# Kernel optimization log

Hardware: AMD Instinct MI355X
Metric: run time of the kernel (lower is better)

Reference implementation:

```python
import jax, jax.numpy as jnp
import numpy as np

V, D = 100000, 300          # fastText vocab / dim
CV, CD, L = 128, 16, 16     # char vocab / char emb dim / word length
F = 50                      # filters per kernel
KS = (3, 4, 5)              # char CNN kernel widths
H = 150                     # LSTM hidden per direction (2H == D)
FH = 150                    # alpha-encoder FFNN hidden
NF, FE = 64, 50             # entity feature vocab / dim
A = 2000                    # num actors
T = 1024                    # tokens
E = 512                     # entity spans
MAXSPAN = 10                # max span length (ragged -> padded+masked)


def setup_inputs() -> dict:
    key = jax.random.key(0)
    ks = jax.random.split(key, 24)
    g = lambda i, shape, s=0.05: jax.random.normal(ks[i], shape, jnp.float32) * s
    inp = {}
    inp['fast_text'] = g(0, (V, D), 0.1)
    inp['actor_matrix'] = g(1, (A, D), 0.1)
    inp['char_table'] = g(2, (CV, CD), 0.1)
    for j, k in enumerate(KS):
        inp[f'conv_w{k}'] = g(3 + j, (F, CD, k))
        inp[f'conv_b{k}'] = jnp.zeros((F,), jnp.float32)
    din = D + F * len(KS)  # 450 = fastText + char features
    inp['Wi_f'] = g(6, (4 * H, din)); inp['Wh_f'] = g(7, (4 * H, H)); inp['b_f'] = jnp.zeros((4 * H,), jnp.float32)
    inp['Wi_b'] = g(8, (4 * H, din)); inp['Wh_b'] = g(9, (4 * H, H)); inp['b_b'] = jnp.zeros((4 * H,), jnp.float32)
    inp['alpha_W1'] = g(10, (D, FH)); inp['alpha_b1'] = jnp.zeros((FH,), jnp.float32)
    inp['alpha_W2'] = g(11, (FH, FH)); inp['alpha_b2'] = jnp.zeros((FH,), jnp.float32)
    inp['alpha_w_out'] = g(12, (FH,))
    inp['feat_table'] = g(13, (NF, FE), 0.1)
    span_dim = 3 * D + 2 * FE  # 1000, per Model1.span_encoding_dim
    inp['affine_W'] = g(14, (span_dim, D)); inp['affine_b'] = jnp.zeros((D,), jnp.float32)
    inp['word_ids'] = jax.random.randint(ks[15], (T,), 0, V)
    inp['char_ids'] = jax.random.randint(ks[16], (T, L), 0, CV)
    starts = jax.random.randint(ks[17], (E,), 0, T - MAXSPAN)
    lens = jax.random.randint(ks[18], (E,), 1, MAXSPAN + 1)
    feats = jax.random.randint(ks[19], (E, 2), 0, NF)
    inp['espans'] = jnp.concatenate([starts[:, None], (starts + lens)[:, None], feats], axis=1)
    return inp


def _renorm(e):
    # nn.Embedding(max_norm=1.0): renormalize looked-up rows to L2 norm <= 1
    n = jnp.linalg.norm(e, axis=-1, keepdims=True)
    return e * jnp.minimum(1.0, 1.0 / jnp.maximum(n, 1e-7))


def _lstm(x, Wi, Wh, b, reverse):
    Hh = Wh.shape[1]
    def step(carry, xt):
        h, c = carry
        z = xt @ Wi.T + h @ Wh.T + b
        i, f, g2, o = jnp.split(z, 4)
        i = jax.nn.sigmoid(i); f = jax.nn.sigmoid(f)
        g2 = jnp.tanh(g2); o = jax.nn.sigmoid(o)
        c = f * c + i * g2
        h = o * jnp.tanh(c)
        return (h, c), h
    init = (jnp.zeros((Hh,), x.dtype), jnp.zeros((Hh,), x.dtype))
    _, hs = jax.lax.scan(step, init, x, reverse=reverse)
    return hs  # [T, H], hs[i] corresponds to position i


def reference(fast_text, actor_matrix, char_table, conv_w3, conv_b3, conv_w4, conv_b4,
              conv_w5, conv_b5, Wi_f, Wh_f, b_f, Wi_b, Wh_b, b_b,
              alpha_W1, alpha_b1, alpha_W2, alpha_b2, alpha_w_out,
              feat_table, affine_W, affine_b, word_ids, char_ids, espans):
    # --- WordEncoder: fastText + char CNN -> BiLSTM contextual embeddings ---
    ft = fast_text[word_ids]                       # [T, D] fastText embeddings (values)
    ce = char_table[char_ids]                      # [T, L, CD]
    xc = jnp.transpose(ce, (0, 2, 1))              # [T, CD, L]
    feats = []
    for w, bb in ((conv_w3, conv_b3), (conv_w4, conv_b4), (conv_w5, conv_b5)):
        y = jax.lax.conv_general_dilated(xc, w, (1,), 'VALID',
                                         dimension_numbers=('NCW', 'OIW', 'NCW'))
        feats.append(jnp.max(jax.nn.relu(y + bb[None, :, None]), axis=-1))  # [T, F]
    char_feat = jnp.concatenate(feats, axis=-1)    # [T, 150]
    lstm_in = jnp.concatenate([ft, char_feat], axis=-1)  # [T, 450]
    h_f = _lstm(lstm_in, Wi_f, Wh_f, b_f, False)
    h_b = _lstm(lstm_in, Wi_b, Wh_b, b_b, True)
    keys = jnp.concatenate([h_f, h_b], axis=-1)    # [T, D] contextual word embeddings
    values = ft

    # --- espan_encodings: ragged span gather, padded + masked, fully vectorized ---
    s, e = espans[:, 0], espans[:, 1]
    fidx = espans[:, 2:]                           # [E, 2]
    offs = jnp.arange(MAXSPAN)
    idx = jnp.clip(s[:, None] + offs[None, :], 0, keys.shape[0] - 1)  # [E, S]
    mask = offs[None, :] < (e - s)[:, None]        # [E, S]
    k_sp = keys[idx]                               # [E, S, D]
    v_sp = values[idx]                             # [E, S, D]
    # SingleQueryEncoder (alpha_encoder): FFNN scores over keys, softmax-pool values
    hsc = jax.nn.relu(k_sp @ alpha_W1 + alpha_b1)
    hsc = jax.nn.relu(hsc @ alpha_W2 + alpha_b2)
    logits = jnp.where(mask, hsc @ alpha_w_out, -1e30)  # [E, S]
    attn = jax.nn.softmax(logits, axis=-1)
    xh = jnp.einsum('es,esd->ed', attn, v_sp)      # [E, D]
    xf = keys[s]                                   # first token
    xl = keys[e - 1]                               # last token
    fs = _renorm(feat_table[fidx]).reshape(fidx.shape[0], -1)  # [E, 2*FE]
    enc = jnp.concatenate([xf, xl, xh, fs], axis=-1)  # [E, 3D+2FE]

    small = enc @ affine_W + affine_b              # [E, D] affine_ent
    actors = _renorm(actor_matrix)                 # [A, D] actor_embedding max_norm=1
    score_link = actors @ small.T                  # [A, E] DotProduct.simpel
    score_1 = jax.nn.logsumexp(score_link, axis=1) # [A]   Maximum.lse over dim=1
    return score_1, score_link
```

## Files before the change

kernel.cpp:

```cpp
#include <hip/hip_runtime.h>
#include <math.h>

typedef _Float16 h2f __attribute__((ext_vector_type(2)));

__device__ __forceinline__ float fdot2f(h2f a, h2f b, float c) {
#if __has_builtin(__builtin_amdgcn_fdot2)
  return __builtin_amdgcn_fdot2(a, b, c, false);
#else
  return c + (float)a[0] * (float)b[0] + (float)a[1] * (float)b[1];
#endif
}

__device__ __forceinline__ float sigf(float x) {
  return __builtin_amdgcn_rcpf(1.f + __expf(-x));
}
__device__ __forceinline__ float tanh_fast(float x) {
  return 2.f * __builtin_amdgcn_rcpf(1.f + __expf(-2.f * x)) - 1.f;
}

__device__ __forceinline__ int clampi(int v, int lo, int hi) {
  return v < lo ? lo : (v > hi ? hi : v);
}

__global__ __launch_bounds__(64) void k_token(
    const float* __restrict__ fast_text, const float* __restrict__ char_table,
    const float* __restrict__ w3, const float* __restrict__ b3,
    const float* __restrict__ w4, const float* __restrict__ b4,
    const float* __restrict__ w5, const float* __restrict__ b5,
    const int* __restrict__ word_ids, const int* __restrict__ char_ids,
    float* __restrict__ lstm_in) {
  const int t = blockIdx.x;
  const int tid = threadIdx.x;
  __shared__ float ce[16][16];
  for (int i = tid; i < 256; i += 64) {
    int l = i >> 4, ci = i & 15;
    ce[l][ci] = char_table[char_ids[t * 16 + l] * 16 + ci];
  }
  __syncthreads();
  const int wid = word_ids[t];
  for (int d = tid; d < 300; d += 64)
    lstm_in[t * 450 + d] = fast_text[wid * 300 + d];
  const int f = tid;
  if (f < 50) {
    {
      float acc[14];
#pragma unroll
      for (int p = 0; p < 14; ++p) acc[p] = 0.f;
      for (int ci = 0; ci < 16; ++ci) {
#pragma unroll
        for (int kk = 0; kk < 3; ++kk) {
          float wv = w3[(f * 16 + ci) * 3 + kk];
#pragma unroll
          for (int p = 0; p < 14; ++p) acc[p] += ce[p + kk][ci] * wv;
        }
      }
      float m = acc[0];
#pragma unroll
      for (int p = 1; p < 14; ++p) m = fmaxf(m, acc[p]);
      lstm_in[t * 450 + 300 + f] = fmaxf(0.f, m + b3[f]);
    }
    {
      float acc[13];
#pragma unroll
      for (int p = 0; p < 13; ++p) acc[p] = 0.f;
      for (int ci = 0; ci < 16; ++ci) {
#pragma unroll
        for (int kk = 0; kk < 4; ++kk) {
          float wv = w4[(f * 16 + ci) * 4 + kk];
#pragma unroll
          for (int p = 0; p < 13; ++p) acc[p] += ce[p + kk][ci] * wv;
        }
      }
      float m = acc[0];
#pragma unroll
      for (int p = 1; p < 13; ++p) m = fmaxf(m, acc[p]);
      lstm_in[t * 450 + 350 + f] = fmaxf(0.f, m + b4[f]);
    }
    {
      float acc[12];
#pragma unroll
      for (int p = 0; p < 12; ++p) acc[p] = 0.f;
      for (int ci = 0; ci < 16; ++ci) {
#pragma unroll
        for (int kk = 0; kk < 5; ++kk) {
          float wv = w5[(f * 16 + ci) * 5 + kk];
#pragma unroll
          for (int p = 0; p < 12; ++p) acc[p] += ce[p + kk][ci] * wv;
        }
      }
      float m = acc[0];
#pragma unroll
      for (int p = 1; p < 12; ++p) m = fmaxf(m, acc[p]);
      lstm_in[t * 450 + 400 + f] = fmaxf(0.f, m + b5[f]);
    }
  }
}

__global__ __launch_bounds__(256) void gemm_nt(
    const float* __restrict__ A, const float* __restrict__ W,
    const float* __restrict__ bias, float* __restrict__ C,
    int M, int N, int K) {
  __shared__ float As[16][64];
  __shared__ float Ws[16][64];
  const int tid = threadIdx.x;
  const int tx = tid & 15, ty = tid >> 4;
  const int r0 = blockIdx.x * 64, c0 = blockIdx.y * 64;
  float acc[4][4] = {};
  for (int k0 = 0; k0 < K; k0 += 16) {
    for (int i = tid; i < 1024; i += 256) {
      int rr = i >> 4, kk = i & 15;
      int r = r0 + rr, k = k0 + kk;
      As[kk][rr] = (r < M && k < K) ? A[r * K + k] : 0.f;
      int c = c0 + rr;
      Ws[kk][rr] = (c < N && k < K) ? W[c * K + k] : 0.f;
    }
    __syncthreads();
#pragma unroll
    for (int kk = 0; kk < 16; ++kk) {
      const float4 av = *(const float4*)(&As[kk][ty * 4]);
      const float4 wv = *(const float4*)(&Ws[kk][tx * 4]);
      float a[4] = {av.x, av.y, av.z, av.w};
      float w[4] = {wv.x, wv.y, wv.z, wv.w};
#pragma unroll
      for (int i = 0; i < 4; ++i)
#pragma unroll
        for (int j = 0; j < 4; ++j) acc[i][j] += a[i] * w[j];
    }
    __syncthreads();
  }
#pragma unroll
  for (int i = 0; i < 4; ++i) {
    int r = r0 + ty * 4 + i;
    if (r >= M) continue;
#pragma unroll
    for (int j = 0; j < 4; ++j) {
      int c = c0 + tx * 4 + j;
      if (c < N) C[r * N + c] = acc[i][j] + (bias ? bias[c] : 0.f);
    }
  }
}

__global__ __launch_bounds__(256) void gemm_xproj(
    const float* __restrict__ A,
    const float* __restrict__ Wf, const float* __restrict__ bf,
    const float* __restrict__ Wb, const float* __restrict__ bb,
    float* __restrict__ xpF, float* __restrict__ xpB) {
  const int M = 1024, N = 600, K = 450;
  const bool back = blockIdx.y >= 10;
  const float* __restrict__ W = back ? Wb : Wf;
  const float* __restrict__ bias = back ? bb : bf;
  float* __restrict__ C = back ? xpB : xpF;
  const int yb = back ? (blockIdx.y - 10) : blockIdx.y;

  __shared__ float As[16][64];
  __shared__ float Ws[16][64];
  const int tid = threadIdx.x;
  const int tx = tid & 15, ty = tid >> 4;
  const int r0 = blockIdx.x * 64, c0 = yb * 64;
  float acc[4][4] = {};
  for (int k0 = 0; k0 < K; k0 += 16) {
    for (int i = tid; i < 1024; i += 256) {
      int rr = i >> 4, kk = i & 15;
      int r = r0 + rr, k = k0 + kk;
      As[kk][rr] = (r < M && k < K) ? A[r * K + k] : 0.f;
      int c = c0 + rr;
      Ws[kk][rr] = (c < N && k < K) ? W[c * K + k] : 0.f;
    }
    __syncthreads();
#pragma unroll
    for (int kk = 0; kk < 16; ++kk) {
      const float4 av = *(const float4*)(&As[kk][ty * 4]);
      const float4 wv = *(const float4*)(&Ws[kk][tx * 4]);
      float a[4] = {av.x, av.y, av.z, av.w};
      float w[4] = {wv.x, wv.y, wv.z, wv.w};
#pragma unroll
      for (int i = 0; i < 4; ++i)
#pragma unroll
        for (int j = 0; j < 4; ++j) acc[i][j] += a[i] * w[j];
    }
    __syncthreads();
  }
#pragma unroll
  for (int i = 0; i < 4; ++i) {
    int r = r0 + ty * 4 + i;
#pragma unroll
    for (int j = 0; j < 4; ++j) {
      int c = c0 + tx * 4 + j;
      if (c < N) C[r * N + c] = acc[i][j] + bias[c];
    }
  }
}

__global__ __launch_bounds__(256, 1) void k_lstm(
    const float* __restrict__ xprojF, const float* __restrict__ xprojB,
    const float* __restrict__ Wh_f, const float* __restrict__ Wh_b,
    float* __restrict__ keys) {
  const int dir = blockIdx.x;
  const float* __restrict__ xp = dir ? xprojB : xprojF;
  const float* __restrict__ Wh = dir ? Wh_b : Wh_f;
  const int tid = threadIdx.x;
  const int i3 = tid < 200 ? tid : 199;
  const int r0 = 3 * i3;

  __shared__ alignas(16) h2f hbuf[2][80];
  __shared__ float zsh[600];

  h2f wA[75], wB[75], wC[75];
  {
    const float2* RA = (const float2*)(Wh + (r0 + 0) * 150);
    const float2* RB = (const float2*)(Wh + (r0 + 1) * 150);
    const float2* RC = (const float2*)(Wh + (r0 + 2) * 150);
#pragma unroll
    for (int kk = 0; kk < 75; ++kk) {
      float2 a = RA[kk], b = RB[kk], d = RC[kk];
      h2f v;
      v[0] = (_Float16)a.x; v[1] = (_Float16)a.y; wA[kk] = v;
      v[0] = (_Float16)b.x; v[1] = (_Float16)b.y; wB[kk] = v;
      v[0] = (_Float16)d.x; v[1] = (_Float16)d.y; wC[kk] = v;
    }
  }
  for (int i = tid; i < 160; i += 256) {
    h2f z;
    z[0] = (_Float16)0.f;
    z[1] = (_Float16)0.f;
    hbuf[i / 80][i % 80] = z;
  }
  float c = 0.f;
  const int t0 = dir ? 1023 : 0;
  float xvA = xp[t0 * 600 + r0 + 0];
  float xvB = xp[t0 * 600 + r0 + 1];
  float xvC = xp[t0 * 600 + r0 + 2];
  __syncthreads();

  int cur = 0;
  for (int step = 0; step < 1024; ++step) {
    const int t = dir ? (1023 - step) : step;
    const int tn = dir ? (t > 0 ? t - 1 : 0) : (t < 1023 ? t + 1 : 1023);
    const float xnA = xp[tn * 600 + r0 + 0];
    const float xnB = xp[tn * 600 + r0 + 1];
    const float xnC = xp[tn * 600 + r0 + 2];
    const float4* hv = (const float4*)hbuf[cur];
    float aA = 0.f, aB = 0.f, aC = 0.f;
#pragma unroll
    for (int q = 0; q < 18; ++q) {
      float4 hq = hv[q];
      const h2f* hh = (const h2f*)&hq;
#pragma unroll
      for (int m = 0; m < 4; ++m) {
        aA = fdot2f(wA[4 * q + m], hh[m], aA);
        aB = fdot2f(wB[4 * q + m], hh[m], aB);
        aC = fdot2f(wC[4 * q + m], hh[m], aC);
      }
    }
    {
      float4 hq = hv[18];
      const h2f* hh = (const h2f*)&hq;
#pragma unroll
      for (int m = 0; m < 3; ++m) {
        aA = fdot2f(wA[72 + m], hh[m], aA);
        aB = fdot2f(wB[72 + m], hh[m], aB);
        aC = fdot2f(wC[72 + m], hh[m], aC);
      }
    }
    if (tid < 200) {
      zsh[r0 + 0] = aA + xvA;
      zsh[r0 + 1] = aB + xvB;
      zsh[r0 + 2] = aC + xvC;
    }
    xvA = xnA; xvB = xnB; xvC = xnC;
    __syncthreads();
    if (tid < 150) {
      const float zi = zsh[tid];
      const float zf = zsh[150 + tid];
      const float zg = zsh[300 + tid];
      const float zo = zsh[450 + tid];
      const float ig = sigf(zi);
      const float fg = sigf(zf);
      const float gg = tanh_fast(zg);
      const float og = sigf(zo);
      c = fg * c + ig * gg;
      const float h = og * tanh_fast(c);
      keys[t * 300 + dir * 150 + tid] = h;
      ((_Float16*)hbuf[cur ^ 1])[tid] = (_Float16)h;
    }
    cur ^= 1;
    __syncthreads();
  }
}

__global__ __launch_bounds__(320) void k_span(
    const float* __restrict__ keys, const float* __restrict__ lstm_in,
    const float* __restrict__ W1, const float* __restrict__ b1,
    const float* __restrict__ W2, const float* __restrict__ b2,
    const float* __restrict__ w_out, const float* __restrict__ feat_table,
    const int* __restrict__ espans, float* __restrict__ enc) {
  const int e = blockIdx.x;
  const int tid = threadIdx.x;
  const int s = espans[e * 4 + 0];
  const int en = espans[e * 4 + 1];
  const int f0 = espans[e * 4 + 2];
  const int f1 = espans[e * 4 + 3];

  __shared__ float ksh[10][300];
  __shared__ float hsh[10][152];
  __shared__ float h2sh[10][152];
  __shared__ float att[10];
  __shared__ float scl[2];

  for (int i = tid; i < 3000; i += 320) {
    int p = i / 300, d = i % 300;
    int row = clampi(s + p, 0, 1023);
    ksh[p][d] = keys[row * 300 + d];
  }
  __syncthreads();

  if (tid < 152) {
    int jj = tid;
    if (jj < 150) {
      float acc[10];
#pragma unroll
      for (int p = 0; p < 10; ++p) acc[p] = b1[jj];
      for (int k = 0; k < 300; k += 4) {
        float w0 = W1[(k + 0) * 150 + jj];
        float w1 = W1[(k + 1) * 150 + jj];
        float w2 = W1[(k + 2) * 150 + jj];
        float w3 = W1[(k + 3) * 150 + jj];
#pragma unroll
        for (int p = 0; p < 10; ++p) {
          const float4 kv = *(const float4*)(&ksh[p][k]);
          acc[p] += kv.x * w0 + kv.y * w1 + kv.z * w2 + kv.w * w3;
        }
      }
#pragma unroll
      for (int p = 0; p < 10; ++p) hsh[p][jj] = fmaxf(acc[p], 0.f);
    } else {
#pragma unroll
      for (int p = 0; p < 10; ++p) hsh[p][jj] = 0.f;
    }
  }
  __syncthreads();

  if (tid < 150) {
    int jj = tid;
    float acc[10];
#pragma unroll
    for (int p = 0; p < 10; ++p) acc[p] = b2[jj];
    for (int k = 0; k < 152; k += 4) {
      float w0 = (k + 0 < 150) ? W2[(k + 0) * 150 + jj] : 0.f;
      float w1 = (k + 1 < 150) ? W2[(k + 1) * 150 + jj] : 0.f;
      float w2 = (k + 2 < 150) ? W2[(k + 2) * 150 + jj] : 0.f;
      float w3 = (k + 3 < 150) ? W2[(k + 3) * 150 + jj] : 0.f;
#pragma unroll
      for (int p = 0; p < 10; ++p) {
        const float4 hv = *(const float4*)(&hsh[p][k]);
        acc[p] += hv.x * w0 + hv.y * w1 + hv.z * w2 + hv.w * w3;
      }
    }
#pragma unroll
    for (int p = 0; p < 10; ++p) h2sh[p][jj] = fmaxf(acc[p], 0.f);
  }
  __syncthreads();

  if (tid < 10) {
    float lg = -1e30f;
    if (tid < en - s) {
      float d = 0.f;
      for (int k = 0; k < 150; ++k) d += h2sh[tid][k] * w_out[k];
      lg = d;
    }
    att[tid] = lg;
  }
  if (tid >= 64 && tid < 66) {
    int r = tid - 64;
    int fi = (r == 0) ? f0 : f1;
    float nsq = 0.f;
    for (int k = 0; k < 50; ++k) {
      float v = feat_table[fi * 50 + k];
      nsq += v * v;
    }
    float n = sqrtf(nsq);
    scl[r] = fminf(1.f, 1.f / fmaxf(n, 1e-7f));
  }
  __syncthreads();

  if (tid == 0) {
    float m = -1e30f;
    for (int p = 0; p < 10; ++p) m = fmaxf(m, att[p]);
    float ex[10];
    float ssum = 0.f;
    for (int p = 0; p < 10; ++p) {
      ex[p] = expf(att[p] - m);
      ssum += ex[p];
    }
    for (int p = 0; p < 10; ++p) att[p] = ex[p] / ssum;
  }
  __syncthreads();

  if (tid < 300) {
    int d = tid;
    float xf = keys[s * 300 + d];
    float xl = keys[(en - 1) * 300 + d];
    float xh = 0.f;
#pragma unroll
    for (int p = 0; p < 10; ++p) {
      int row = clampi(s + p, 0, 1023);
      xh += att[p] * lstm_in[row * 450 + d];
    }
    enc[e * 1000 + d] = xf;
    enc[e * 1000 + 300 + d] = xl;
    enc[e * 1000 + 600 + d] = xh;
  }
  if (tid < 100) {
    int r = tid / 50, cc = tid % 50;
    int fi = (r == 0) ? f0 : f1;
    enc[e * 1000 + 900 + tid] = feat_table[fi * 50 + cc] * scl[r];
  }
}

__global__ __launch_bounds__(320) void k_affine(
    const float* __restrict__ enc, const float* __restrict__ W,
    const float* __restrict__ bias, float* __restrict__ small) {
  const int e0 = blockIdx.x * 4;
  const int tid = threadIdx.x;
  __shared__ float es[4][1000];
  for (int i = tid; i < 4000; i += 320) es[i / 1000][i % 1000] = enc[e0 * 1000 + i];
  __syncthreads();
  if (tid < 300) {
    float a0 = bias[tid], a1 = bias[tid], a2 = bias[tid], a3 = bias[tid];
    for (int k = 0; k < 1000; k += 4) {
      float w0 = W[(k + 0) * 300 + tid];
      float w1 = W[(k + 1) * 300 + tid];
      float w2 = W[(k + 2) * 300 + tid];
      float w3 = W[(k + 3) * 300 + tid];
      const float4 v0 = *(const float4*)(&es[0][k]);
      const float4 v1 = *(const float4*)(&es[1][k]);
      const float4 v2 = *(const float4*)(&es[2][k]);
      const float4 v3 = *(const float4*)(&es[3][k]);
      a0 += v0.x * w0 + v0.y * w1 + v0.z * w2 + v0.w * w3;
      a1 += v1.x * w0 + v1.y * w1 + v1.z * w2 + v1.w * w3;
      a2 += v2.x * w0 + v2.y * w1 + v2.z * w2 + v2.w * w3;
      a3 += v3.x * w0 + v3.y * w1 + v3.z * w2 + v3.w * w3;
    }
    small[(e0 + 0) * 300 + tid] = a0;
    small[(e0 + 1) * 300 + tid] = a1;
    small[(e0 + 2) * 300 + tid] = a2;
    small[(e0 + 3) * 300 + tid] = a3;
  }
}

__global__ __launch_bounds__(64) void k_renorm(
    const float* __restrict__ actors, float* __restrict__ actorsN) {
  const int a = blockIdx.x;
  const int l = threadIdx.x;
  float nsq = 0.f;
  for (int d = l; d < 300; d += 64) {
    float v = actors[a * 300 + d];
    nsq += v * v;
  }
  for (int off = 32; off; off >>= 1) nsq += __shfl_down(nsq, off);
  nsq = __shfl(nsq, 0);
  float sc = fminf(1.f, 1.f / fmaxf(sqrtf(nsq), 1e-7f));
  for (int d = l; d < 300; d += 64) actorsN[a * 300 + d] = actors[a * 300 + d] * sc;
}

__global__ __launch_bounds__(64) void k_lse(
    const float* __restrict__ link, float* __restrict__ out) {
  const int a = blockIdx.x;
  const int l = threadIdx.x;
  float v[8];
  float m = -1e30f;
#pragma unroll
  for (int i = 0; i < 8; ++i) {
    v[i] = link[a * 512 + l + i * 64];
    m = fmaxf(m, v[i]);
  }
  for (int off = 32; off; off >>= 1) m = fmaxf(m, __shfl_xor(m, off));
  float ssum = 0.f;
#pragma unroll
  for (int i = 0; i < 8; ++i) ssum += expf(v[i] - m);
  for (int off = 32; off; off >>= 1) ssum += __shfl_xor(ssum, off);
  if (l == 0) out[a] = logf(ssum) + m;
}

extern "C" void kernel_launch(void* const* d_in, const int* in_sizes, int n_in,
                              void* d_out, int out_size, void* d_ws, size_t ws_size,
                              hipStream_t stream) {
  const float* fast_text = (const float*)d_in[0];
  const float* actor_matrix = (const float*)d_in[1];
  const float* char_table = (const float*)d_in[2];
  const float* w3 = (const float*)d_in[3];
  const float* b3 = (const float*)d_in[4];
  const float* w4 = (const float*)d_in[5];
  const float* b4 = (const float*)d_in[6];
  const float* w5 = (const float*)d_in[7];
  const float* b5 = (const float*)d_in[8];
  const float* Wi_f = (const float*)d_in[9];
  const float* Wh_f = (const float*)d_in[10];
  const float* b_f = (const float*)d_in[11];
  const float* Wi_b = (const float*)d_in[12];
  const float* Wh_b = (const float*)d_in[13];
  const float* b_b = (const float*)d_in[14];
  const float* alpha_W1 = (const float*)d_in[15];
  const float* alpha_b1 = (const float*)d_in[16];
  const float* alpha_W2 = (const float*)d_in[17];
  const float* alpha_b2 = (const float*)d_in[18];
  const float* alpha_w_out = (const float*)d_in[19];
  const float* feat_table = (const float*)d_in[20];
  const float* affine_W = (const float*)d_in[21];
  const float* affine_b = (const float*)d_in[22];
  const int* word_ids = (const int*)d_in[23];
  const int* char_ids = (const int*)d_in[24];
  const int* espans = (const int*)d_in[25];

  float* ws = (float*)d_ws;
  float* lstm_in = ws;
  float* xpF = lstm_in + 460800;
  float* xpB = xpF + 614400;
  float* keys = xpB + 614400;
  float* enc = keys + 307200;
  float* small = enc + 512000;
  float* actN = small + 153600;

  float* out = (float*)d_out;
  float* score_link = out + 2000;

  k_token<<<1024, 64, 0, stream>>>(fast_text, char_table, w3, b3, w4, b4, w5, b5,
                                   word_ids, char_ids, lstm_in);
  gemm_xproj<<<dim3(16, 20), 256, 0, stream>>>(lstm_in, Wi_f, b_f, Wi_b, b_b,
                                               xpF, xpB);
  k_lstm<<<2, 256, 0, stream>>>(xpF, xpB, Wh_f, Wh_b, keys);
  k_renorm<<<2000, 64, 0, stream>>>(actor_matrix, actN);
  k_span<<<512, 320, 0, stream>>>(keys, lstm_in, alpha_W1, alpha_b1, alpha_W2,
                                  alpha_b2, alpha_w_out, feat_table, espans, enc);
  k_affine<<<128, 320, 0, stream>>>(enc, affine_W, affine_b, small);
  gemm_nt<<<dim3(32, 8), 256, 0, stream>>>(actN, small, nullptr, score_link,
                                           2000, 512, 300);
  k_lse<<<2000, 64, 0, stream>>>(score_link, out);
}
```

Measured before the change: 1.183 ms.

## Split LSTM recurrent matvec across 4-lane groups with DPP reduction

Each thread in the recurrent LSTM kernel used to compute three full gate rows over all 150 hidden inputs. Now groups of 4 lanes share 10 rows, each lane covering a 40-element slice of K, and the partial sums are combined with DPP cross-lane adds. This cuts the per-thread serial dot-product chain on the per-step critical path and uses all 256 threads. The cost is extra DPP shuffles, a remapped shared-memory gate layout, and some redundant padded work.

```diff
diff --git a/kernel.cpp b/kernel.cpp
--- a/kernel.cpp
+++ b/kernel.cpp
@@ -9,6 +9,14 @@
 #else
   return c + (float)a[0] * (float)b[0] + (float)a[1] * (float)b[1];
 #endif
+}
+
+template <int CTRL>
+__device__ __forceinline__ float dpp_f(float x) {
+  union { float f; int i; } u, r;
+  u.f = x;
+  r.i = __builtin_amdgcn_update_dpp(0, u.i, CTRL, 0xF, 0xF, false);
+  return r.f;
 }
 
 __device__ __forceinline__ float sigf(float x) {
@@ -199,81 +207,124 @@
   const float* __restrict__ xp = dir ? xprojB : xprojF;
   const float* __restrict__ Wh = dir ? Wh_b : Wh_f;
   const int tid = threadIdx.x;
-  const int i3 = tid < 200 ? tid : 199;
-  const int r0 = 3 * i3;
+  const int g = tid & 3;
+  const int b = tid >> 2;
 
   __shared__ alignas(16) h2f hbuf[2][80];
-  __shared__ float zsh[600];
-
-  h2f wA[75], wB[75], wC[75];
-  {
-    const float2* RA = (const float2*)(Wh + (r0 + 0) * 150);
-    const float2* RB = (const float2*)(Wh + (r0 + 1) * 150);
-    const float2* RC = (const float2*)(Wh + (r0 + 2) * 150);
-#pragma unroll
-    for (int kk = 0; kk < 75; ++kk) {
-      float2 a = RA[kk], b = RB[kk], d = RC[kk];
-      h2f v;
-      v[0] = (_Float16)a.x; v[1] = (_Float16)a.y; wA[kk] = v;
-      v[0] = (_Float16)b.x; v[1] = (_Float16)b.y; wB[kk] = v;
-      v[0] = (_Float16)d.x; v[1] = (_Float16)d.y; wC[kk] = v;
-    }
-  }
+  __shared__ float zsh[10][64];
+
+  h2f w0[20], w1[20], w2[20], w3[20], w4[20];
+  h2f w5[20], w6[20], w7[20], w8[20], w9[20];
+#define LOADROW(WARR, R)                                              \
+  {                                                                   \
+    const int row_ = 10 * b + (R);                                    \
+    const float* Rp_ = Wh + (row_ < 600 ? row_ : 599) * 150;          \
+    _Pragma("unroll") for (int kk = 0; kk < 20; ++kk) {               \
+      const int k_ = 40 * g + 2 * kk;                                 \
+      float x0_ = 0.f, x1_ = 0.f;                                     \
+      if (k_ < 150) {                                                 \
+        float2 p_ = *(const float2*)(Rp_ + k_);                       \
+        x0_ = p_.x;                                                   \
+        x1_ = p_.y;                                                   \
+      }                                                               \
+      h2f v_;                                                         \
+      v_[0] = (_Float16)x0_;                                          \
+      v_[1] = (_Float16)x1_;                                          \
+      WARR[kk] = v_;                                                  \
+    }                                                                 \
+  }
+  LOADROW(w0, 0) LOADROW(w1, 1) LOADROW(w2, 2) LOADROW(w3, 3) LOADROW(w4, 4)
+  LOADROW(w5, 5) LOADROW(w6, 6) LOADROW(w7, 7) LOADROW(w8, 8) LOADROW(w9, 9)
+#undef LOADROW
+
   for (int i = tid; i < 160; i += 256) {
     h2f z;
     z[0] = (_Float16)0.f;
     z[1] = (_Float16)0.f;
     hbuf[i / 80][i % 80] = z;
   }
+
+  const int wr0 = clampi(10 * b + g, 0, 599);
+  const int wr1 = clampi(10 * b + g + 4, 0, 599);
+  const int wr2 = clampi(10 * b + g + 8, 0, 599);
+
+  int go0 = 0, go1 = 0, go2 = 0, go3 = 0;
+  if (tid < 150) {
+    const int r0_ = tid, r1_ = tid + 150, r2_ = tid + 300, r3_ = tid + 450;
+    go0 = (r0_ % 10) * 64 + r0_ / 10;
+    go1 = (r1_ % 10) * 64 + r1_ / 10;
+    go2 = (r2_ % 10) * 64 + r2_ / 10;
+    go3 = (r3_ % 10) * 64 + r3_ / 10;
+  }
+
   float c = 0.f;
   const int t0 = dir ? 1023 : 0;
-  float xvA = xp[t0 * 600 + r0 + 0];
-  float xvB = xp[t0 * 600 + r0 + 1];
-  float xvC = xp[t0 * 600 + r0 + 2];
+  float xv0 = xp[t0 * 600 + wr0];
+  float xv1 = xp[t0 * 600 + wr1];
+  float xv2 = xp[t0 * 600 + wr2];
   __syncthreads();
 
   int cur = 0;
   for (int step = 0; step < 1024; ++step) {
     const int t = dir ? (1023 - step) : step;
     const int tn = dir ? (t > 0 ? t - 1 : 0) : (t < 1023 ? t + 1 : 1023);
-    const float xnA = xp[tn * 600 + r0 + 0];
-    const float xnB = xp[tn * 600 + r0 + 1];
-    const float xnC = xp[tn * 600 + r0 + 2];
-    const float4* hv = (const float4*)hbuf[cur];
-    float aA = 0.f, aB = 0.f, aC = 0.f;
-#pragma unroll
-    for (int q = 0; q < 18; ++q) {
-      float4 hq = hv[q];
-      const h2f* hh = (const h2f*)&hq;
-#pragma unroll
-      for (int m = 0; m < 4; ++m) {
-        aA = fdot2f(wA[4 * q + m], hh[m], aA);
-        aB = fdot2f(wB[4 * q + m], hh[m], aB);
-        aC = fdot2f(wC[4 * q + m], hh[m], aC);
-      }
-    }
-    {
-      float4 hq = hv[18];
-      const h2f* hh = (const h2f*)&hq;
-#pragma unroll
-      for (int m = 0; m < 3; ++m) {
-        aA = fdot2f(wA[72 + m], hh[m], aA);
-        aB = fdot2f(wB[72 + m], hh[m], aB);
-        aC = fdot2f(wC[72 + m], hh[m], aC);
-      }
-    }
-    if (tid < 200) {
-      zsh[r0 + 0] = aA + xvA;
-      zsh[r0 + 1] = aB + xvB;
-      zsh[r0 + 2] = aC + xvC;
-    }
-    xvA = xnA; xvB = xnB; xvC = xnC;
+    const float xn0 = xp[tn * 600 + wr0];
+    const float xn1 = xp[tn * 600 + wr1];
+    const float xn2 = xp[tn * 600 + wr2];
+    const float4* hv = (const float4*)hbuf[cur] + 5 * g;
+    float4 q0 = hv[0], q1 = hv[1], q2 = hv[2], q3 = hv[3], q4 = hv[4];
+    float a[10];
+#pragma unroll
+    for (int r = 0; r < 10; ++r) a[r] = 0.f;
+#define DOTC(Q, KB)                                                   \
+  {                                                                   \
+    const h2f* hh_ = (const h2f*)&Q;                                  \
+    _Pragma("unroll") for (int m = 0; m < 4; ++m) {                   \
+      const h2f hk_ = hh_[m];                                         \
+      a[0] = fdot2f(w0[(KB) + m], hk_, a[0]);                         \
+      a[1] = fdot2f(w1[(KB) + m], hk_, a[1]);                         \
+      a[2] = fdot2f(w2[(KB) + m], hk_, a[2]);                         \
+      a[3] = fdot2f(w3[(KB) + m], hk_, a[3]);                         \
+      a[4] = fdot2f(w4[(KB) + m], hk_, a[4]);                         \
+      a[5] = fdot2f(w5[(KB) + m], hk_, a[5]);                         \
+      a[6] = fdot2f(w6[(KB) + m], hk_, a[6]);                         \
+      a[7] = fdot2f(w7[(KB) + m], hk_, a[7]);                         \
+      a[8] = fdot2f(w8[(KB) + m], hk_, a[8]);                         \
+      a[9] = fdot2f(w9[(KB) + m], hk_, a[9]);                         \
+    }                                                                 \
+  }
+    DOTC(q0, 0) DOTC(q1, 4) DOTC(q2, 8) DOTC(q3, 12) DOTC(q4, 16)
+#undef DOTC
+#pragma unroll
+    for (int r = 0; r < 10; ++r) {
+      const float e = a[r] + dpp_f<0xB1>(a[r]);
+      a[r] = e + dpp_f<0x4E>(e);
+    }
+    if (g == 0) {
+      zsh[0][b] = a[0] + xv0;
+      zsh[4][b] = a[4] + xv1;
+      zsh[8][b] = a[8] + xv2;
+    } else if (g == 1) {
+      zsh[1][b] = a[1] + xv0;
+      zsh[5][b] = a[5] + xv1;
+      zsh[9][b] = a[9] + xv2;
+    } else if (g == 2) {
+      zsh[2][b] = a[2] + xv0;
+      zsh[6][b] = a[6] + xv1;
+    } else {
+      zsh[3][b] = a[3] + xv0;
+      zsh[7][b] = a[7] + xv1;
+    }
+    xv0 = xn0;
+    xv1 = xn1;
+    xv2 = xn2;
     __syncthreads();
     if (tid < 150) {
-      const float zi = zsh[tid];
-      const float zf = zsh[150 + tid];
-      const float zg = zsh[300 + tid];
-      const float zo = zsh[450 + tid];
+      const float* zf_ = (const float*)zsh;
+      const float zi = zf_[go0];
+      const float zf = zf_[go1];
+      const float zg = zf_[go2];
+      const float zo = zf_[go3];
       const float ig = sigf(zi);
       const float fg = sigf(zf);
       const float gg = tanh_fast(zg);
```

Result: slower. 1.222 ms (+3.3%).
